# Kernel tuning notes

Measured on AMD Instinct MI355X. Metric: run time of the kernel, lower is better.

Reference implementation:

```python
import math
import jax, jax.numpy as jnp
import numpy as np

N_EMBD = 1024
N_HEAD = 16
B, T = 4, 2048


def _layernorm(x, g, b, eps=1e-5):
    mu = jnp.mean(x, axis=-1, keepdims=True)
    var = jnp.var(x, axis=-1, keepdims=True)
    return (x - mu) * jax.lax.rsqrt(var + eps) * g + b


def _causal_attn(x, wq, bq, wk, bk, wv, bv, wo, bo):
    Bq, Tq, C = x.shape
    H = N_HEAD
    Dh = C // H
    q = (jnp.einsum('btc,cd->btd', x, wq) + bq).reshape(Bq, Tq, H, Dh)
    k = (jnp.einsum('btc,cd->btd', x, wk) + bk).reshape(Bq, Tq, H, Dh)
    v = (jnp.einsum('btc,cd->btd', x, wv) + bv).reshape(Bq, Tq, H, Dh)
    att = jnp.einsum('bqhd,bkhd->bhqk', q, k) * (1.0 / math.sqrt(Dh))
    causal = jnp.tril(jnp.ones((Tq, Tq), dtype=bool))
    att = jnp.where(causal[None, None], att, -jnp.inf)
    att = jax.nn.softmax(att, axis=-1)
    y = jnp.einsum('bhqk,bkhd->bqhd', att, v).reshape(Bq, Tq, C)
    return jnp.einsum('btc,cd->btd', y, wo) + bo


def _mlp(x, w1, b1, w2, b2):
    h = jax.nn.gelu(jnp.einsum('btc,cf->btf', x, w1) + b1, approximate=False)
    return jnp.einsum('btf,fc->btc', h, w2) + b2


def setup_inputs() -> dict:
    key = jax.random.key(0)
    ks = jax.random.split(key, 32)
    C, F = N_EMBD, 4 * N_EMBD
    s = 0.02
    d = {'x': jax.random.normal(ks[0], (B, T, C), jnp.float32)}
    i = 1
    for a in ('a1', 'a2'):
        for n in ('wq', 'wk', 'wv', 'wo'):
            d[f'{a}_{n}'] = jax.random.normal(ks[i], (C, C), jnp.float32) * s; i += 1
            d[f'{a}_{n[1:]and "b"+n[1]}'] = jnp.zeros((C,), jnp.float32)
    for m in ('m1', 'm2'):
        d[f'{m}_w1'] = jax.random.normal(ks[i], (C, F), jnp.float32) * s; i += 1
        d[f'{m}_b1'] = jnp.zeros((F,), jnp.float32)
        d[f'{m}_w2'] = jax.random.normal(ks[i], (F, C), jnp.float32) * s; i += 1
        d[f'{m}_b2'] = jnp.zeros((C,), jnp.float32)
    for ln in ('ln1', 'ln2', 'ln3', 'ln4'):
        d[f'{ln}_g'] = jnp.ones((C,), jnp.float32)
        d[f'{ln}_b'] = jnp.zeros((C,), jnp.float32)
    # fix attention bias names: a1_bq etc.
    for a in ('a1', 'a2'):
        for hn in ('bq', 'bk', 'bv', 'bo'):
            d[f'{a}_{hn}'] = jnp.zeros((C,), jnp.float32)
    return d


def reference(x,
              a1_wq, a1_bq, a1_wk, a1_bk, a1_wv, a1_bv, a1_wo, a1_bo,
              a2_wq, a2_bq, a2_wk, a2_bk, a2_wv, a2_bv, a2_wo, a2_bo,
              m1_w1, m1_b1, m1_w2, m1_b2,
              m2_w1, m2_b1, m2_w2, m2_b2,
              ln1_g, ln1_b, ln2_g, ln2_b, ln3_g, ln3_b, ln4_g, ln4_b,
              **_ignored):
    x = x + _causal_attn(_layernorm(x, ln1_g, ln1_b),
                         a1_wq, a1_bq, a1_wk, a1_bk, a1_wv, a1_bv, a1_wo, a1_bo)
    x = x + _mlp(_layernorm(x, ln2_g, ln2_b), m1_w1, m1_b1, m1_w2, m1_b2)
    x = x + _causal_attn(_layernorm(x, ln3_g, ln3_b),
                         a2_wq, a2_bq, a2_wk, a2_bk, a2_wv, a2_bv, a2_wo, a2_bo)
    x = x + _mlp(_layernorm(x, ln4_g, ln4_b), m2_w1, m2_b1, m2_w2, m2_b2)
    return x
```

## Files before the change

### kernel.cpp

```cpp
#include <hip/hip_runtime.h>


typedef short bf16x8 __attribute__((ext_vector_type(8)));
typedef float f32x4 __attribute__((ext_vector_type(4)));
typedef unsigned int u32;

#define MFMA16(a, b, c) __builtin_amdgcn_mfma_f32_16x16x32_bf16(a, b, c, 0, 0, 0)
#define SCHED_FENCE() __builtin_amdgcn_sched_barrier(0)

__device__ __forceinline__ unsigned short f2bf(float f) {
  union { float f; unsigned int u; } v; v.f = f;
  unsigned int u = v.u;
  return (unsigned short)((u + 0x7FFFu + ((u >> 16) & 1u)) >> 16);
}

__device__ __forceinline__ unsigned short f2bf_fast(float f) {
  union { float f; unsigned int u; } v; v.f = f;
  return (unsigned short)((v.u + 0x8000u) >> 16);
}

__device__ __forceinline__ float bf2f(unsigned short u) {
  union { unsigned int u; float f; } v; v.u = ((unsigned int)u) << 16;
  return v.f;
}

__device__ __forceinline__ void async16(const void* g, void* l) {
  __builtin_amdgcn_global_load_lds(
      (__attribute__((address_space(1))) void*)(g),
      (__attribute__((address_space(3))) void*)(l), 16, 0, 0);
}

__global__ __launch_bounds__(256) void transpose_cvt(
    const float* __restrict__ W, unsigned short* __restrict__ Wt, int K, int N) {
  __shared__ float t[32][33];
  int n0 = blockIdx.x * 32, k0 = blockIdx.y * 32;
  int tx = threadIdx.x, ty = threadIdx.y;
#pragma unroll
  for (int j = 0; j < 4; ++j)
    t[ty + 8 * j][tx] = W[(size_t)(k0 + ty + 8 * j) * N + n0 + tx];
  __syncthreads();
#pragma unroll
  for (int j = 0; j < 4; ++j)
    Wt[(size_t)(n0 + ty + 8 * j) * K + k0 + tx] = f2bf(t[tx][ty + 8 * j]);
}

__global__ void concat3(const float* __restrict__ a, const float* __restrict__ b,
                        const float* __restrict__ c, float* __restrict__ o) {
  int i = blockIdx.x * 256 + threadIdx.x;
  if (i < 1024) o[i] = a[i];
  else if (i < 2048) o[i] = b[i - 1024];
  else if (i < 3072) o[i] = c[i - 2048];
}

__global__ __launch_bounds__(256) void ln_kernel(
    const float* __restrict__ x, const float* __restrict__ g,
    const float* __restrict__ b, unsigned short* __restrict__ out) {
  int row = blockIdx.x;
  int tid = threadIdx.x;
  float4 v = ((const float4*)(x + (size_t)row * 1024))[tid];
  float s = v.x + v.y + v.z + v.w;
  float ss = v.x * v.x + v.y * v.y + v.z * v.z + v.w * v.w;
#pragma unroll
  for (int m = 1; m < 64; m <<= 1) {
    s += __shfl_xor(s, m);
    ss += __shfl_xor(ss, m);
  }
  __shared__ float red[8];
  int wid = tid >> 6, lane = tid & 63;
  if (lane == 0) { red[wid] = s; red[4 + wid] = ss; }
  __syncthreads();
  s = red[0] + red[1] + red[2] + red[3];
  ss = red[4] + red[5] + red[6] + red[7];
  float mean = s * (1.f / 1024.f);
  float var = ss * (1.f / 1024.f) - mean * mean;
  float rstd = rsqrtf(var + 1e-5f);
  float4 gv = ((const float4*)g)[tid];
  float4 bv = ((const float4*)b)[tid];
  ushort4 o;
  o.x = f2bf((v.x - mean) * rstd * gv.x + bv.x);
  o.y = f2bf((v.y - mean) * rstd * gv.y + bv.y);
  o.z = f2bf((v.z - mean) * rstd * gv.z + bv.z);
  o.w = f2bf((v.w - mean) * rstd * gv.w + bv.w);
  ((ushort4*)(out + (size_t)row * 1024))[tid] = o;
}

template <int MODE>
__global__ __launch_bounds__(256) void gemm_kernel(
    const unsigned short* __restrict__ A, const unsigned short* __restrict__ Bt,
    const float* __restrict__ bias, const float* resid, void* out,
    int M, int N, int K, int nbn) {
  __shared__ unsigned short As[128 * 64];
  __shared__ unsigned short Bs[128 * 64];

  int nwg = gridDim.x;
  int bid = blockIdx.x;
  int swz = (bid & 7) * (nwg >> 3) + (bid >> 3);
  int bm = swz / nbn, bn = swz % nbn;

  int tid = threadIdx.x;
  int wid = tid >> 6, lane = tid & 63;
  int wr = wid >> 1, wc = wid & 1;
  int fr = lane & 15, fg = lane >> 4;
  int srow = tid >> 3, scs = tid & 7;

  const size_t abase = (size_t)(bm * 128) * K;
  const size_t bbase = (size_t)(bn * 128) * K;

  f32x4 acc[4][4] = {};

  for (int kt = 0; kt < K; kt += 64) {
    __syncthreads();
#pragma unroll
    for (int i = 0; i < 4; ++i) {
      int row = i * 32 + srow;
      int c = scs ^ (row & 7);
      async16(A + abase + (size_t)row * K + kt + 8 * c, As + i * 2048 + wid * 512);
    }
#pragma unroll
    for (int i = 0; i < 4; ++i) {
      int row = i * 32 + srow;
      int c = scs ^ (row & 7);
      async16(Bt + bbase + (size_t)row * K + kt + 8 * c, Bs + i * 2048 + wid * 512);
    }
    __syncthreads();
#pragma unroll
    for (int ks = 0; ks < 2; ++ks) {
      bf16x8 af[4], bf[4];
#pragma unroll
      for (int f = 0; f < 4; ++f) {
        int ra = wr * 64 + f * 16 + fr;
        int ca = (ks * 4 + fg) ^ (ra & 7);
        af[f] = *(const bf16x8*)(As + ra * 64 + ca * 8);
        int rb = wc * 64 + f * 16 + fr;
        int cb = (ks * 4 + fg) ^ (rb & 7);
        bf[f] = *(const bf16x8*)(Bs + rb * 64 + cb * 8);
      }
#pragma unroll
      for (int a = 0; a < 4; ++a)
#pragma unroll
        for (int b2 = 0; b2 < 4; ++b2)
          acc[a][b2] = MFMA16(af[a], bf[b2], acc[a][b2]);
    }
  }

  int m0 = bm * 128 + wr * 64, n0 = bn * 128 + wc * 64;
#pragma unroll
  for (int a = 0; a < 4; ++a) {
#pragma unroll
    for (int b2 = 0; b2 < 4; ++b2) {
      int n = n0 + b2 * 16 + fr;
      float bsv = bias[n];
#pragma unroll
      for (int r = 0; r < 4; ++r) {
        int m = m0 + a * 16 + fg * 4 + r;
        float v = acc[a][b2][r] + bsv;
        if (MODE == 0) {
          ((unsigned short*)out)[(size_t)m * N + n] = f2bf(v);
        } else if (MODE == 1) {
          v = 0.5f * v * (1.0f + erff(v * 0.70710678118654752f));
          ((unsigned short*)out)[(size_t)m * N + n] = f2bf(v);
        } else {
          ((float*)out)[(size_t)m * N + n] = resid[(size_t)m * N + n] + v;
        }
      }
    }
  }
}

template <int MODE>
__global__ __launch_bounds__(512, 2) void gemm256(
    const unsigned short* __restrict__ A, const unsigned short* __restrict__ Bt,
    const float* __restrict__ bias, const float* resid, void* out,
    int M, int N, int K, int nbn) {
  __shared__ unsigned short As[2][256 * 64];
  __shared__ unsigned short Bs[2][256 * 64];

  int nwg = gridDim.x;
  int bid = blockIdx.x;
  int swz = (bid & 7) * (nwg >> 3) + (bid >> 3);
  int bm = swz / nbn, bn = swz % nbn;

  int tid = threadIdx.x;
  int wid = tid >> 6, lane = tid & 63;
  int wm = wid >> 2, wn = wid & 3;
  int fr = lane & 15, fg = lane >> 4;
  int srow = tid >> 3, su = tid & 7;
  int sc = su ^ (srow & 7);

  const size_t abase = (size_t)(bm * 256) * K;
  const size_t bbase = (size_t)(bn * 256) * K;

  f32x4 acc[8][4] = {};

  auto STAGE = [&](int pp, int kt) {
#pragma unroll
    for (int i = 0; i < 4; ++i)
      async16(A + abase + (size_t)(i * 64 + srow) * K + kt + sc * 8,
              &As[pp][i * 4096 + tid * 8]);
#pragma unroll
    for (int i = 0; i < 4; ++i)
      async16(Bt + bbase + (size_t)(i * 64 + srow) * K + kt + sc * 8,
              &Bs[pp][i * 4096 + tid * 8]);
  };

  const int NT = K >> 6;
  STAGE(0, 0);

  for (int kt = 0; kt < NT; ++kt) {
    int p = kt & 1;
    if (kt + 1 < NT) {
      STAGE(p ^ 1, (kt + 1) * 64);
      asm volatile("s_waitcnt vmcnt(8)" ::: "memory");
    } else {
      asm volatile("s_waitcnt vmcnt(0)" ::: "memory");
    }
    SCHED_FENCE();
    __builtin_amdgcn_s_barrier();
    SCHED_FENCE();

    bf16x8 bfr[4][2];
#pragma unroll
    for (int n = 0; n < 4; ++n)
#pragma unroll
      for (int ks = 0; ks < 2; ++ks)
        bfr[n][ks] = *(const bf16x8*)(
            &Bs[p][(wn * 64 + n * 16 + fr) * 64 + ((ks * 4 + fg) ^ (fr & 7)) * 8]);
#pragma unroll
    for (int qm = 0; qm < 2; ++qm) {
      bf16x8 afr[4][2];
#pragma unroll
      for (int a = 0; a < 4; ++a)
#pragma unroll
        for (int ks = 0; ks < 2; ++ks)
          afr[a][ks] = *(const bf16x8*)(
              &As[p][(wm * 128 + qm * 64 + a * 16 + fr) * 64 + ((ks * 4 + fg) ^ (fr & 7)) * 8]);
      __builtin_amdgcn_s_setprio(1);
#pragma unroll
      for (int ks = 0; ks < 2; ++ks)
#pragma unroll
        for (int a = 0; a < 4; ++a)
#pragma unroll
          for (int n = 0; n < 4; ++n)
            acc[qm * 4 + a][n] = MFMA16(afr[a][ks], bfr[n][ks], acc[qm * 4 + a][n]);
      __builtin_amdgcn_s_setprio(0);
    }

    SCHED_FENCE();
    __builtin_amdgcn_s_barrier();
    SCHED_FENCE();
  }

  int m0 = bm * 256 + wm * 128, n0 = bn * 256 + wn * 64;
#pragma unroll
  for (int a = 0; a < 8; ++a) {
#pragma unroll
    for (int n = 0; n < 4; ++n) {
      int col = n0 + n * 16 + fr;
      float bsv = bias[col];
#pragma unroll
      for (int r = 0; r < 4; ++r) {
        int row = m0 + a * 16 + fg * 4 + r;
        float v = acc[a][n][r] + bsv;
        if (MODE == 0) {
          ((unsigned short*)out)[(size_t)row * N + col] = f2bf(v);
        } else if (MODE == 1) {
          v = 0.5f * v * (1.0f + erff(v * 0.70710678118654752f));
          ((unsigned short*)out)[(size_t)row * N + col] = f2bf(v);
        } else {
          ((float*)out)[(size_t)row * N + col] = resid[(size_t)row * N + col] + v;
        }
      }
    }
  }
}

__global__ __launch_bounds__(256) void attn_kernel(
    const unsigned short* __restrict__ qkv, unsigned short* __restrict__ y) {
  __shared__ unsigned short Ks[2][64 * 64];
  __shared__ unsigned short Vt[2][64 * 72];
  __shared__ u32 Pf[4][16 * 36];

  int qt = 31 - (int)blockIdx.x;
  int bh = blockIdx.y;
  int b = bh >> 4, h = bh & 15;
  int tid = threadIdx.x, wid = tid >> 6, lane = tid & 63;
  int fr = lane & 15, fg = lane >> 4;

  const unsigned short* qp = qkv + (size_t)(b * 2048) * 3072 + h * 64;
  const unsigned short* kp = qp + 1024;
  const unsigned short* vp = qp + 2048;

  int qrow = qt * 64 + wid * 16 + fr;
  const unsigned short* qrp = qp + (size_t)qrow * 3072;
  bf16x8 qf[2];
#pragma unroll
  for (int ks = 0; ks < 2; ++ks) {
    bf16x8 raw = *(const bf16x8*)(qrp + ks * 32 + 8 * fg);
#pragma unroll
    for (int j = 0; j < 8; ++j)
      qf[ks][j] = (short)f2bf(bf2f((unsigned short)raw[j]) * 0.125f);
  }

  float rs = 0.f;
  f32x4 oacc[4] = {};

  int kvp = tid & 31, dgrp = tid >> 5;

  auto stageK = [&](int t, int p) {
#pragma unroll
    for (int i = 0; i < 2; ++i) {
      int row = i * 32 + (tid >> 3);
      int c = (tid & 7) ^ (row & 7);
      async16(kp + (size_t)(t * 64 + row) * 3072 + 8 * c, &Ks[p][i * 2048 + tid * 8]);
    }
  };
  bf16x8 rva, rvb;
  auto loadV = [&](int t) {
    const unsigned short* v0 = vp + (size_t)(t * 64 + 2 * kvp) * 3072 + 8 * dgrp;
    rva = *(const bf16x8*)v0;
    rvb = *(const bf16x8*)(v0 + 3072);
  };

  stageK(0, 0);
  loadV(0);

  for (int t = 0; t <= qt; ++t) {
    int p = t & 1;
    if (t < qt) stageK(t + 1, p ^ 1);
    {
      u32* base = (u32*)Vt[p];
#pragma unroll
      for (int j = 0; j < 8; ++j)
        base[(8 * dgrp + j) * 36 + kvp] =
            (u32)(unsigned short)rva[j] | ((u32)(unsigned short)rvb[j] << 16);
    }
    asm volatile("s_waitcnt vmcnt(4)" ::: "memory");
    asm volatile("s_waitcnt lgkmcnt(0)" ::: "memory");
    SCHED_FENCE();
    __builtin_amdgcn_s_barrier();
    SCHED_FENCE();
    if (t < qt) loadV(t + 1);

    f32x4 s[4];
    __builtin_amdgcn_s_setprio(1);
#pragma unroll
    for (int n = 0; n < 4; ++n) {
      s[n] = (f32x4){0.f, 0.f, 0.f, 0.f};
#pragma unroll
      for (int ks = 0; ks < 2; ++ks) {
        int row = n * 16 + fr;
        int cs = (ks * 4 + fg) ^ (row & 7);
        bf16x8 kf = *(const bf16x8*)(&Ks[p][row * 64 + cs * 8]);
        s[n] = MFMA16(kf, qf[ks], s[n]);
      }
    }
    __builtin_amdgcn_s_setprio(0);

    if (t == qt) {
#pragma unroll
      for (int n = 0; n < 4; ++n)
#pragma unroll
        for (int r = 0; r < 4; ++r)
          if (n * 16 + fg * 4 + r > wid * 16 + fr) s[n][r] = -1e30f;
    }

    u32* Pw = Pf[wid];
#pragma unroll
    for (int n = 0; n < 4; ++n) {
      float p0 = __expf(s[n][0]), p1 = __expf(s[n][1]);
      float p2 = __expf(s[n][2]), p3 = __expf(s[n][3]);
      rs += (p0 + p1) + (p2 + p3);
      Pw[fr * 36 + 8 * n + 2 * fg + 0] = (u32)f2bf_fast(p0) | ((u32)f2bf_fast(p1) << 16);
      Pw[fr * 36 + 8 * n + 2 * fg + 1] = (u32)f2bf_fast(p2) | ((u32)f2bf_fast(p3) << 16);
    }

    bf16x8 pa[2];
    pa[0] = *(const bf16x8*)(Pw + fr * 36 + 0 * 16 + fg * 4);
    pa[1] = *(const bf16x8*)(Pw + fr * 36 + 1 * 16 + fg * 4);

    __builtin_amdgcn_s_setprio(1);
#pragma unroll
    for (int db = 0; db < 4; ++db)
#pragma unroll
      for (int ks = 0; ks < 2; ++ks) {
        bf16x8 vf = *(const bf16x8*)(&Vt[p][(db * 16 + fr) * 72 + ks * 32 + 8 * fg]);
        oacc[db] = MFMA16(pa[ks], vf, oacc[db]);
      }
    __builtin_amdgcn_s_setprio(0);

    SCHED_FENCE();
    __builtin_amdgcn_s_barrier();
    SCHED_FENCE();
  }

  float rt = rs;
  rt += __shfl_xor(rt, 16);
  rt += __shfl_xor(rt, 32);
  unsigned short* yp = y + (size_t)(b * 2048 + qt * 64 + wid * 16) * 1024 + h * 64;
#pragma unroll
  for (int r = 0; r < 4; ++r) {
    float dn = __shfl(rt, fg * 4 + r);
    float inv = 1.0f / dn;
#pragma unroll
    for (int db = 0; db < 4; ++db)
      yp[(size_t)(fg * 4 + r) * 1024 + db * 16 + fr] = f2bf(oacc[db][r] * inv);
  }
}

extern "C" void kernel_launch(void* const* d_in, const int* in_sizes, int n_in,
                              void* d_out, int out_size, void* d_ws, size_t ws_size,
                              hipStream_t stream) {
  (void)in_sizes; (void)n_in; (void)out_size; (void)ws_size;
  char* ws = (char*)d_ws;
  unsigned short* ACT1 = (unsigned short*)(ws);
  unsigned short* ACT2 = (unsigned short*)(ws + 16777216);
  unsigned short* WQKV1 = (unsigned short*)(ws + 83886080);
  unsigned short* WO1   = (unsigned short*)(ws + 90177536);
  unsigned short* WQKV2 = (unsigned short*)(ws + 92274688);
  unsigned short* WO2   = (unsigned short*)(ws + 98566144);
  unsigned short* WF1_1 = (unsigned short*)(ws + 100663296);
  unsigned short* WF2_1 = (unsigned short*)(ws + 109051904);
  unsigned short* WF1_2 = (unsigned short*)(ws + 117440512);
  unsigned short* WF2_2 = (unsigned short*)(ws + 125829120);
  float* BQKV1 = (float*)(ws + 134217728);
  float* BQKV2 = (float*)(ws + 134230016);

  const float* x = (const float*)d_in[0];
  float* OUT = (float*)d_out;

  auto T = [&](int idx, unsigned short* dst, int K, int N) {
    transpose_cvt<<<dim3(N / 32, K / 32), dim3(32, 8), 0, stream>>>(
        (const float*)d_in[idx], dst, K, N);
  };
  T(1, WQKV1, 1024, 1024); T(3, WQKV1 + 1024 * 1024, 1024, 1024);
  T(5, WQKV1 + 2 * 1024 * 1024, 1024, 1024); T(7, WO1, 1024, 1024);
  T(9, WQKV2, 1024, 1024); T(11, WQKV2 + 1024 * 1024, 1024, 1024);
  T(13, WQKV2 + 2 * 1024 * 1024, 1024, 1024); T(15, WO2, 1024, 1024);
  T(17, WF1_1, 1024, 4096); T(19, WF2_1, 4096, 1024);
  T(21, WF1_2, 1024, 4096); T(23, WF2_2, 4096, 1024);
  concat3<<<12, 256, 0, stream>>>((const float*)d_in[2], (const float*)d_in[4],
                                  (const float*)d_in[6], BQKV1);
  concat3<<<12, 256, 0, stream>>>((const float*)d_in[10], (const float*)d_in[12],
                                  (const float*)d_in[14], BQKV2);

  auto LN = [&](const float* in, int gi, int bi) {
    ln_kernel<<<8192, 256, 0, stream>>>(in, (const float*)d_in[gi],
                                        (const float*)d_in[bi], ACT1);
  };
  auto G = [&](int mode, const unsigned short* A, const unsigned short* Bt,
               const float* bias, const float* resid, void* out, int N, int K) {
    int nbn = N / 128;
    int nwg = 64 * nbn;
    if (mode == 0)
      gemm_kernel<0><<<nwg, 256, 0, stream>>>(A, Bt, bias, resid, out, 8192, N, K, nbn);
    else if (mode == 1)
      gemm_kernel<1><<<nwg, 256, 0, stream>>>(A, Bt, bias, resid, out, 8192, N, K, nbn);
    else
      gemm_kernel<2><<<nwg, 256, 0, stream>>>(A, Bt, bias, resid, out, 8192, N, K, nbn);
  };
  auto G256 = [&](int mode, const unsigned short* A, const unsigned short* Bt,
                  const float* bias, const float* resid, void* out, int N, int K) {
    int nbn = N / 256;
    int nwg = 32 * nbn;
    if (mode == 0)
      gemm256<0><<<nwg, 512, 0, stream>>>(A, Bt, bias, resid, out, 8192, N, K, nbn);
    else if (mode == 1)
      gemm256<1><<<nwg, 512, 0, stream>>>(A, Bt, bias, resid, out, 8192, N, K, nbn);
    else
      gemm256<2><<<nwg, 512, 0, stream>>>(A, Bt, bias, resid, out, 8192, N, K, nbn);
  };

  LN(x, 25, 26);
  G256(0, ACT1, WQKV1, BQKV1, nullptr, ACT2, 3072, 1024);
  attn_kernel<<<dim3(32, 64), 256, 0, stream>>>(ACT2, ACT1);
  G(2, ACT1, WO1, (const float*)d_in[8], x, OUT, 1024, 1024);
  LN(OUT, 27, 28);
  G256(1, ACT1, WF1_1, (const float*)d_in[18], nullptr, ACT2, 4096, 1024);
  G(2, ACT2, WF2_1, (const float*)d_in[20], OUT, OUT, 1024, 4096);
  LN(OUT, 29, 30);
  G256(0, ACT1, WQKV2, BQKV2, nullptr, ACT2, 3072, 1024);
  attn_kernel<<<dim3(32, 64), 256, 0, stream>>>(ACT2, ACT1);
  G(2, ACT1, WO2, (const float*)d_in[16], OUT, OUT, 1024, 1024);
  LN(OUT, 31, 32);
  G256(1, ACT1, WF1_2, (const float*)d_in[22], nullptr, ACT2, 4096, 1024);
  G(2, ACT2, WF2_2, (const float*)d_in[24], OUT, OUT, 1024, 4096);
}
```

Measured before the change: 1.125 ms.

## Pair causal query tiles per 512-thread block and use exp2/packed bf16 conversion

The attention kernel now runs 8 waves per block over 128-row query tiles. Each block processes two query tiles (pr and 15-pr), so every block does about the same amount of causal work, and the K/V tiles staged in LDS are shared by twice as many query rows. Waves skip KV tiles that lie entirely above their causal diagonal. The softmax uses raw v_exp_f32, with log2e folded into the Q scale, and converts pairs to bf16 with the hardware v_cvt_pk_bf16_f32 instruction. The costs are fewer, larger blocks (512 in total), sequential processing of the two phases, and divergent per-wave skipping that still has to meet every barrier.

New measurement: 1.085 ms. -3.6%, faster.

```diff
diff --git a/kernel.cpp b/kernel.cpp
--- a/kernel.cpp
+++ b/kernel.cpp
@@ -14,14 +14,21 @@
   return (unsigned short)((u + 0x7FFFu + ((u >> 16) & 1u)) >> 16);
 }
 
-__device__ __forceinline__ unsigned short f2bf_fast(float f) {
-  union { float f; unsigned int u; } v; v.f = f;
-  return (unsigned short)((v.u + 0x8000u) >> 16);
-}
-
 __device__ __forceinline__ float bf2f(unsigned short u) {
   union { unsigned int u; float f; } v; v.u = ((unsigned int)u) << 16;
   return v.f;
+}
+
+__device__ __forceinline__ float exp2_raw(float x) {
+  float r;
+  asm("v_exp_f32 %0, %1" : "=v"(r) : "v"(x));
+  return r;
+}
+
+__device__ __forceinline__ u32 cvt_pk_bf16(float a, float b) {
+  u32 r;
+  asm("v_cvt_pk_bf16_f32 %0, %1, %2" : "=v"(r) : "v"(a), "v"(b));
+  return r;
 }
 
 __device__ __forceinline__ void async16(const void* g, void* l) {
@@ -274,13 +281,13 @@
   }
 }
 
-__global__ __launch_bounds__(256) void attn_kernel(
+__global__ __launch_bounds__(512) void attn_kernel(
     const unsigned short* __restrict__ qkv, unsigned short* __restrict__ y) {
   __shared__ unsigned short Ks[2][64 * 64];
   __shared__ unsigned short Vt[2][64 * 72];
-  __shared__ u32 Pf[4][16 * 36];
-
-  int qt = 31 - (int)blockIdx.x;
+  __shared__ u32 Pf[8][16 * 36];
+
+  int pr = blockIdx.x;
   int bh = blockIdx.y;
   int b = bh >> 4, h = bh & 15;
   int tid = threadIdx.x, wid = tid >> 6, lane = tid & 63;
@@ -290,120 +297,124 @@
   const unsigned short* kp = qp + 1024;
   const unsigned short* vp = qp + 2048;
 
-  int qrow = qt * 64 + wid * 16 + fr;
-  const unsigned short* qrp = qp + (size_t)qrow * 3072;
-  bf16x8 qf[2];
-#pragma unroll
-  for (int ks = 0; ks < 2; ++ks) {
-    bf16x8 raw = *(const bf16x8*)(qrp + ks * 32 + 8 * fg);
-#pragma unroll
-    for (int j = 0; j < 8; ++j)
-      qf[ks][j] = (short)f2bf(bf2f((unsigned short)raw[j]) * 0.125f);
-  }
-
-  float rs = 0.f;
-  f32x4 oacc[4] = {};
-
-  int kvp = tid & 31, dgrp = tid >> 5;
+  int krow = tid >> 3;
+  int kcs = (tid & 7) ^ (krow & 7);
+  int kvp = tid & 31, dg4 = tid >> 5;
 
   auto stageK = [&](int t, int p) {
-#pragma unroll
-    for (int i = 0; i < 2; ++i) {
-      int row = i * 32 + (tid >> 3);
-      int c = (tid & 7) ^ (row & 7);
-      async16(kp + (size_t)(t * 64 + row) * 3072 + 8 * c, &Ks[p][i * 2048 + tid * 8]);
-    }
-  };
-  bf16x8 rva, rvb;
+    async16(kp + (size_t)(t * 64 + krow) * 3072 + 8 * kcs, &Ks[p][tid * 8]);
+  };
+  ushort4 rva, rvb;
   auto loadV = [&](int t) {
-    const unsigned short* v0 = vp + (size_t)(t * 64 + 2 * kvp) * 3072 + 8 * dgrp;
-    rva = *(const bf16x8*)v0;
-    rvb = *(const bf16x8*)(v0 + 3072);
-  };
-
-  stageK(0, 0);
-  loadV(0);
-
-  for (int t = 0; t <= qt; ++t) {
-    int p = t & 1;
-    if (t < qt) stageK(t + 1, p ^ 1);
-    {
-      u32* base = (u32*)Vt[p];
+    const unsigned short* v0 = vp + (size_t)(t * 64 + 2 * kvp) * 3072 + 4 * dg4;
+    rva = *(const ushort4*)v0;
+    rvb = *(const ushort4*)(v0 + 3072);
+  };
+
+  for (int ph = 0; ph < 2; ++ph) {
+    int qt = ph == 0 ? pr : 15 - pr;
+    int nkv = 2 * qt + 2;
+    int q0 = qt * 128 + wid * 16;
+
+    const unsigned short* qrp = qp + (size_t)(q0 + fr) * 3072;
+    bf16x8 qf[2];
+#pragma unroll
+    for (int ks = 0; ks < 2; ++ks) {
+      bf16x8 raw = *(const bf16x8*)(qrp + ks * 32 + 8 * fg);
 #pragma unroll
       for (int j = 0; j < 8; ++j)
-        base[(8 * dgrp + j) * 36 + kvp] =
-            (u32)(unsigned short)rva[j] | ((u32)(unsigned short)rvb[j] << 16);
-    }
-    asm volatile("s_waitcnt vmcnt(4)" ::: "memory");
-    asm volatile("s_waitcnt lgkmcnt(0)" ::: "memory");
-    SCHED_FENCE();
-    __builtin_amdgcn_s_barrier();
-    SCHED_FENCE();
-    if (t < qt) loadV(t + 1);
-
-    f32x4 s[4];
-    __builtin_amdgcn_s_setprio(1);
-#pragma unroll
-    for (int n = 0; n < 4; ++n) {
-      s[n] = (f32x4){0.f, 0.f, 0.f, 0.f};
-#pragma unroll
-      for (int ks = 0; ks < 2; ++ks) {
-        int row = n * 16 + fr;
-        int cs = (ks * 4 + fg) ^ (row & 7);
-        bf16x8 kf = *(const bf16x8*)(&Ks[p][row * 64 + cs * 8]);
-        s[n] = MFMA16(kf, qf[ks], s[n]);
+        qf[ks][j] = (short)f2bf(bf2f((unsigned short)raw[j]) * 0.18033688011112042f);
+    }
+
+    float rs = 0.f;
+    f32x4 oacc[4] = {};
+
+    stageK(0, 0);
+    loadV(0);
+
+    for (int t = 0; t < nkv; ++t) {
+      int p = t & 1;
+      if (t + 1 < nkv) stageK(t + 1, p ^ 1);
+      {
+        u32* base = (u32*)Vt[p];
+#pragma unroll
+        for (int j = 0; j < 4; ++j)
+          base[(4 * dg4 + j) * 36 + kvp] =
+              (u32)rva[j] | ((u32)rvb[j] << 16);
       }
-    }
-    __builtin_amdgcn_s_setprio(0);
-
-    if (t == qt) {
-#pragma unroll
-      for (int n = 0; n < 4; ++n)
-#pragma unroll
-        for (int r = 0; r < 4; ++r)
-          if (n * 16 + fg * 4 + r > wid * 16 + fr) s[n][r] = -1e30f;
-    }
-
-    u32* Pw = Pf[wid];
-#pragma unroll
-    for (int n = 0; n < 4; ++n) {
-      float p0 = __expf(s[n][0]), p1 = __expf(s[n][1]);
-      float p2 = __expf(s[n][2]), p3 = __expf(s[n][3]);
-      rs += (p0 + p1) + (p2 + p3);
-      Pw[fr * 36 + 8 * n + 2 * fg + 0] = (u32)f2bf_fast(p0) | ((u32)f2bf_fast(p1) << 16);
-      Pw[fr * 36 + 8 * n + 2 * fg + 1] = (u32)f2bf_fast(p2) | ((u32)f2bf_fast(p3) << 16);
-    }
-
-    bf16x8 pa[2];
-    pa[0] = *(const bf16x8*)(Pw + fr * 36 + 0 * 16 + fg * 4);
-    pa[1] = *(const bf16x8*)(Pw + fr * 36 + 1 * 16 + fg * 4);
-
-    __builtin_amdgcn_s_setprio(1);
-#pragma unroll
-    for (int db = 0; db < 4; ++db)
-#pragma unroll
-      for (int ks = 0; ks < 2; ++ks) {
-        bf16x8 vf = *(const bf16x8*)(&Vt[p][(db * 16 + fr) * 72 + ks * 32 + 8 * fg]);
-        oacc[db] = MFMA16(pa[ks], vf, oacc[db]);
+      asm volatile("s_waitcnt lgkmcnt(0)" ::: "memory");
+      SCHED_FENCE();
+      __builtin_amdgcn_s_barrier();
+      SCHED_FENCE();
+      if (t + 1 < nkv) loadV(t + 1);
+
+      int kv0 = t * 64;
+      if (kv0 <= q0 + 15) {
+        f32x4 s[4];
+        __builtin_amdgcn_s_setprio(1);
+#pragma unroll
+        for (int n = 0; n < 4; ++n) {
+          s[n] = (f32x4){0.f, 0.f, 0.f, 0.f};
+#pragma unroll
+          for (int ks = 0; ks < 2; ++ks) {
+            int row = n * 16 + fr;
+            int cs = (ks * 4 + fg) ^ (row & 7);
+            bf16x8 kf = *(const bf16x8*)(&Ks[p][row * 64 + cs * 8]);
+            s[n] = MFMA16(kf, qf[ks], s[n]);
+          }
+        }
+        __builtin_amdgcn_s_setprio(0);
+
+        if (kv0 + 63 > q0) {
+#pragma unroll
+          for (int n = 0; n < 4; ++n)
+#pragma unroll
+            for (int r = 0; r < 4; ++r)
+              if (kv0 + n * 16 + fg * 4 + r > q0 + fr) s[n][r] = -1e30f;
+        }
+
+        u32* Pw = Pf[wid];
+#pragma unroll
+        for (int n = 0; n < 4; ++n) {
+          float p0 = exp2_raw(s[n][0]), p1 = exp2_raw(s[n][1]);
+          float p2 = exp2_raw(s[n][2]), p3 = exp2_raw(s[n][3]);
+          rs += (p0 + p1) + (p2 + p3);
+          Pw[fr * 36 + 8 * n + 2 * fg + 0] = cvt_pk_bf16(p0, p1);
+          Pw[fr * 36 + 8 * n + 2 * fg + 1] = cvt_pk_bf16(p2, p3);
+        }
+
+        bf16x8 pa[2];
+        pa[0] = *(const bf16x8*)(Pw + fr * 36 + 0 * 16 + fg * 4);
+        pa[1] = *(const bf16x8*)(Pw + fr * 36 + 1 * 16 + fg * 4);
+
+        __builtin_amdgcn_s_setprio(1);
+#pragma unroll
+        for (int db = 0; db < 4; ++db)
+#pragma unroll
+          for (int ks = 0; ks < 2; ++ks) {
+            bf16x8 vf = *(const bf16x8*)(&Vt[p][(db * 16 + fr) * 72 + ks * 32 + 8 * fg]);
+            oacc[db] = MFMA16(pa[ks], vf, oacc[db]);
+          }
+        __builtin_amdgcn_s_setprio(0);
       }
-    __builtin_amdgcn_s_setprio(0);
-
-    SCHED_FENCE();
-    __builtin_amdgcn_s_barrier();
-    SCHED_FENCE();
-  }
-
-  float rt = rs;
-  rt += __shfl_xor(rt, 16);
-  rt += __shfl_xor(rt, 32);
-  unsigned short* yp = y + (size_t)(b * 2048 + qt * 64 + wid * 16) * 1024 + h * 64;
-#pragma unroll
-  for (int r = 0; r < 4; ++r) {
-    float dn = __shfl(rt, fg * 4 + r);
-    float inv = 1.0f / dn;
-#pragma unroll
-    for (int db = 0; db < 4; ++db)
-      yp[(size_t)(fg * 4 + r) * 1024 + db * 16 + fr] = f2bf(oacc[db][r] * inv);
+
+      SCHED_FENCE();
+      __builtin_amdgcn_s_barrier();
+      SCHED_FENCE();
+    }
+
+    float rt = rs;
+    rt += __shfl_xor(rt, 16);
+    rt += __shfl_xor(rt, 32);
+    unsigned short* yp = y + (size_t)(b * 2048 + q0) * 1024 + h * 64;
+#pragma unroll
+    for (int r = 0; r < 4; ++r) {
+      float dn = __shfl(rt, fg * 4 + r);
+      float inv = 1.0f / dn;
+#pragma unroll
+      for (int db = 0; db < 4; ++db)
+        yp[(size_t)(fg * 4 + r) * 1024 + db * 16 + fr] = f2bf(oacc[db][r] * inv);
+    }
   }
 }
 
@@ -472,14 +483,14 @@
 
   LN(x, 25, 26);
   G256(0, ACT1, WQKV1, BQKV1, nullptr, ACT2, 3072, 1024);
-  attn_kernel<<<dim3(32, 64), 256, 0, stream>>>(ACT2, ACT1);
+  attn_kernel<<<dim3(8, 64), 512, 0, stream>>>(ACT2, ACT1);
   G(2, ACT1, WO1, (const float*)d_in[8], x, OUT, 1024, 1024);
   LN(OUT, 27, 28);
   G256(1, ACT1, WF1_1, (const float*)d_in[18], nullptr, ACT2, 4096, 1024);
   G(2, ACT2, WF2_1, (const float*)d_in[20], OUT, OUT, 1024, 4096);
   LN(OUT, 29, 30);
   G256(0, ACT1, WQKV2, BQKV2, nullptr, ACT2, 3072, 1024);
-  attn_kernel<<<dim3(32, 64), 256, 0, stream>>>(ACT2, ACT1);
+  attn_kernel<<<dim3(8, 64), 512, 0, stream>>>(ACT2, ACT1);
   G(2, ACT1, WO2, (const float*)d_in[16], OUT, OUT, 1024, 1024);
   LN(OUT, 31, 32);
   G256(1, ACT1, WF1_2, (const float*)d_in[22], nullptr, ACT2, 4096, 1024);
```
